# Performance work log

Measured on AMD Instinct MI355X. Metric: run time of the kernel, lower is better.

## Reference

```python
import jax, jax.numpy as jnp
import numpy as np
import math

B, L, HID = 2, 2048, 1024
NH, DH = 16, 64
MASK_VAL = -1000000000.0  # half_precision_flag == False


def setup_inputs() -> dict:
    key = jax.random.key(0)
    ks = jax.random.split(key, 12)
    s = 0.02
    return {
        "queries": jax.random.normal(ks[0], (B, L, HID), jnp.float32),
        "keys": jax.random.normal(ks[1], (B, L, HID), jnp.float32),
        "values": jax.random.normal(ks[2], (B, L, HID), jnp.float32),
        "mask": jax.random.randint(ks[3], (B, L, L), 0, 2, jnp.int32),
        "Wq": jax.random.normal(ks[4], (HID, NH * DH), jnp.float32) * s,
        "bq": jnp.zeros((NH * DH,), jnp.float32),
        "Wk": jax.random.normal(ks[5], (HID, NH * DH), jnp.float32) * s,
        "bk": jnp.zeros((NH * DH,), jnp.float32),
        "Wv": jax.random.normal(ks[6], (HID, NH * DH), jnp.float32) * s,
        "bv": jnp.zeros((NH * DH,), jnp.float32),
        "Wo": jax.random.normal(ks[7], (NH * DH, HID), jnp.float32) * s,
        "bo": jnp.zeros((HID,), jnp.float32),
    }


def reference(queries, keys, values, mask, Wq, bq, Wk, bk, Wv, bv, Wo, bo):
    # Linear projections: (B, L, NH*DH)
    q = queries @ Wq + bq
    k = keys @ Wk + bk
    v = values @ Wv + bv
    # FAITHFUL to original: raw .view(B, NH, -1, DH) without transpose
    q = q.reshape(B, NH, L, DH)
    k = k.reshape(B, NH, L, DH)
    v = v.reshape(B, NH, L, DH)
    # scaled dot-product scores: (B, NH, L, L)
    scores = jnp.einsum("bhqd,bhkd->bhqk", q, k) / math.sqrt(DH)
    scores = jnp.where(mask[:, None, :, :] == 0, MASK_VAL, scores)
    probs = jax.nn.softmax(scores, axis=-1)  # dropout p=0 -> identity
    ctx = jnp.einsum("bhqk,bhkd->bhqd", probs, v)  # (B, NH, L, DH)
    # transpose(1,2) then flatten heads, as in original
    ctx = ctx.transpose(0, 2, 1, 3).reshape(B, L, NH * DH)
    return ctx @ Wo + bo
```

## Files before the change

### kernel.cpp

```cpp
#include <hip/hip_runtime.h>
#include <stdint.h>

typedef __bf16 bf16;
typedef __bf16 bf16x8 __attribute__((ext_vector_type(8)));
typedef __bf16 bf16x4 __attribute__((ext_vector_type(4)));
typedef __bf16 bf16x2 __attribute__((ext_vector_type(2)));
typedef float  f32x4  __attribute__((ext_vector_type(4)));
typedef float  f32x16 __attribute__((ext_vector_type(16)));
typedef short  s16x4  __attribute__((ext_vector_type(4)));
typedef short  s16x8  __attribute__((ext_vector_type(8)));
typedef unsigned int u32x2 __attribute__((ext_vector_type(2)));
typedef unsigned int u32x4 __attribute__((ext_vector_type(4)));
typedef unsigned long long ull;

#define GLOAD16(gptr, lptr)                                                     \
  __builtin_amdgcn_global_load_lds(                                             \
      (const __attribute__((address_space(1))) void*)(gptr),                    \
      (__attribute__((address_space(3))) void*)(lptr), 16, 0, 0)

#define MFMA16(a, b, c) __builtin_amdgcn_mfma_f32_16x16x32_bf16((a), (b), (c), 0, 0, 0)
#define MFMA32(a, b, c) __builtin_amdgcn_mfma_f32_32x32x16_bf16((a), (b), (c), 0, 0, 0)

static constexpr int B_ = 2, L_ = 2048, NH_ = 16, DH_ = 64;
static constexpr float QSCALE = 0.18033688011112042f;

__global__ __launch_bounds__(256) void k_prep(const float* __restrict__ q,
                                              const float* __restrict__ k,
                                              const float* __restrict__ v,
                                              const int* __restrict__ mask,
                                              const float* __restrict__ wq,
                                              const float* __restrict__ wk,
                                              const float* __restrict__ wv,
                                              const float* __restrict__ wo,
                                              bf16* __restrict__ X,
                                              bf16* __restrict__ Wt,
                                              ull* __restrict__ mb) {
  __shared__ float t[32][33];
  const int bid = blockIdx.x, tid = threadIdx.x;
  if (bid < 32768) {
    int tt = bid * 256 + tid;
    ull bal = __ballot(mask[tt] != 0);
    if ((tid & 63) == 0) mb[tt >> 6] = bal;
  } else if (bid < 45056) {
    int u = bid - 32768;
    int z = u >> 12, x = u & 4095;
    const float* in = z == 0 ? q : (z == 1 ? k : v);
    bf16* out = X + (size_t)z * 4194304;
    int i = x * 256 + tid;
    const float4 f = ((const float4*)in)[i];
    bf16x4 o = {(bf16)f.x, (bf16)f.y, (bf16)f.z, (bf16)f.w};
    ((bf16x4*)out)[i] = o;
  } else {
    int u = bid - 45056;
    int z = u >> 10, rem = u & 1023;
    const float* in = z == 0 ? wq : (z == 1 ? wk : (z == 2 ? wv : wo));
    bf16* out = Wt + (size_t)z * 1048576;
    int bx = (rem & 31) * 32, by = (rem >> 5) * 32;
    int x = tid & 31, y = tid >> 5;
#pragma unroll
    for (int r = 0; r < 4; ++r)
      t[y + r * 8][x] = in[(size_t)(by + y + r * 8) * 1024 + bx + x];
    __syncthreads();
#pragma unroll
    for (int r = 0; r < 4; ++r)
      out[(size_t)(bx + y + r * 8) * 1024 + by + x] = (bf16)t[x][y + r * 8];
  }
}

__global__ __launch_bounds__(256) void k_gemm3(const bf16* __restrict__ Xb,
                                               const bf16* __restrict__ Wb,
                                               const float* __restrict__ b0,
                                               const float* __restrict__ b1,
                                               const float* __restrict__ b2,
                                               bf16* __restrict__ Ob) {
  const int z = blockIdx.z;
  const bf16* A  = Xb + (size_t)z * 4194304;
  const bf16* Bt = Wb + (size_t)z * 1048576;
  const float* bias = z == 0 ? b0 : (z == 1 ? b1 : b2);
  bf16* C = Ob + (size_t)z * 4194304;
  const int m0 = blockIdx.y * 128, n0 = blockIdx.x * 128;
  __shared__ __align__(16) bf16 As[128 * 32];
  __shared__ __align__(16) bf16 Bs[128 * 32];
  const int tid = threadIdx.x, lane = tid & 63, w = tid >> 6, quad = lane >> 4, l15 = lane & 15;
  const int wm = (w & 1) * 64, wn = (w >> 1) * 64;
  f32x4 acc[4][4] = {};
  for (int kt = 0; kt < 32; ++kt) {
    const int kk = kt * 32;
#pragma unroll
    for (int i = 0; i < 2; ++i) {
      int s = tid + i * 256;
      int r = s >> 2, c = (s & 3) ^ ((r >> 1) & 3);
      GLOAD16(A + (size_t)(m0 + r) * 1024 + kk + c * 8, As + s * 8);
      GLOAD16(Bt + (size_t)(n0 + r) * 1024 + kk + c * 8, Bs + s * 8);
    }
    __syncthreads();
    bf16x8 af[4], bb[4];
#pragma unroll
    for (int i = 0; i < 4; ++i) {
      int ra = wm + i * 16 + l15, rb = wn + i * 16 + l15;
      af[i] = *(const bf16x8*)(As + (ra * 4 + (quad ^ ((ra >> 1) & 3))) * 8);
      bb[i] = *(const bf16x8*)(Bs + (rb * 4 + (quad ^ ((rb >> 1) & 3))) * 8);
    }
#pragma unroll
    for (int mi = 0; mi < 4; ++mi)
#pragma unroll
      for (int ni = 0; ni < 4; ++ni)
        acc[mi][ni] = MFMA16(af[mi], bb[ni], acc[mi][ni]);
    __syncthreads();
  }
  const float scale = (z == 0) ? QSCALE : 1.0f;
#pragma unroll
  for (int mi = 0; mi < 4; ++mi)
#pragma unroll
    for (int ni = 0; ni < 4; ++ni) {
      int row = m0 + wm + mi * 16 + quad * 4;
      int col = n0 + wn + ni * 16 + l15;
      float bz = bias[col];
      if (z == 2) {
        int b_ = row >> 11, l = row & 2047;
        int hh = l >> 7;
        int i0 = (l & 127) * 16 + (col >> 6);
        int d  = col & 63;
        bf16* dst = C + (size_t)(b_ * 16 + hh) * 131072;
#pragma unroll
        for (int r = 0; r < 4; ++r) {
          int iK = i0 + 16 * r;
          dst[((size_t)(iK >> 3) * 64 + d) * 8 + (iK & 7)] = (bf16)(acc[mi][ni][r] + bz);
        }
      } else {
#pragma unroll
        for (int r = 0; r < 4; ++r)
          C[(size_t)(row + r) * 1024 + col] = (bf16)((acc[mi][ni][r] + bz) * scale);
      }
    }
}

__global__ __launch_bounds__(256) void k_gemmo(const bf16* __restrict__ A,
                                               const bf16* __restrict__ Bt,
                                               const float* __restrict__ bias,
                                               float* __restrict__ C) {
  const int m0 = blockIdx.y * 64, n0 = blockIdx.x * 128;
  __shared__ __align__(16) bf16 As[64 * 32];
  __shared__ __align__(16) bf16 Bs[128 * 32];
  const int tid = threadIdx.x, lane = tid & 63, w = tid >> 6, quad = lane >> 4, l15 = lane & 15;
  const int wn = w * 32;
  f32x4 acc[4][2] = {};
  for (int kt = 0; kt < 32; ++kt) {
    const int kk = kt * 32;
    {
      int r = tid >> 2, c = (tid & 3) ^ ((r >> 1) & 3);
      GLOAD16(A + (size_t)(m0 + r) * 1024 + kk + c * 8, As + tid * 8);
    }
#pragma unroll
    for (int i = 0; i < 2; ++i) {
      int s = tid + i * 256;
      int r = s >> 2, c = (s & 3) ^ ((r >> 1) & 3);
      GLOAD16(Bt + (size_t)(n0 + r) * 1024 + kk + c * 8, Bs + s * 8);
    }
    __syncthreads();
    bf16x8 af[4], bb[2];
#pragma unroll
    for (int i = 0; i < 4; ++i) {
      int ra = i * 16 + l15;
      af[i] = *(const bf16x8*)(As + (ra * 4 + (quad ^ ((ra >> 1) & 3))) * 8);
    }
#pragma unroll
    for (int i = 0; i < 2; ++i) {
      int rb = wn + i * 16 + l15;
      bb[i] = *(const bf16x8*)(Bs + (rb * 4 + (quad ^ ((rb >> 1) & 3))) * 8);
    }
#pragma unroll
    for (int mi = 0; mi < 4; ++mi)
#pragma unroll
      for (int ni = 0; ni < 2; ++ni)
        acc[mi][ni] = MFMA16(af[mi], bb[ni], acc[mi][ni]);
    __syncthreads();
  }
#pragma unroll
  for (int mi = 0; mi < 4; ++mi)
#pragma unroll
    for (int ni = 0; ni < 2; ++ni) {
      int row = m0 + mi * 16 + quad * 4;
      int col = n0 + wn + ni * 16 + l15;
      float bz = bias[col];
#pragma unroll
      for (int r = 0; r < 4; ++r)
        C[(size_t)(row + r) * 1024 + col] = acc[mi][ni][r] + bz;
    }
}

static __device__ __forceinline__ unsigned pack2(float a, float b) {
  bf16x2 t = {(bf16)a, (bf16)b};
  return __builtin_bit_cast(unsigned, t);
}

static __device__ __forceinline__ void flash_step(
    const bf16* __restrict__ Kc, const bf16* __restrict__ Vc, ull word,
    const bf16x8 (&qf)[4], bf16x8 ones8,
    int hi, int keyq, int vo0, int vo1, int vo2, int vo3,
    f32x16& accO0, f32x16& accO1, f32x16& accL) {
  bf16x8 v0 = *(const bf16x8*)(Vc + vo0);
  bf16x8 v1 = *(const bf16x8*)(Vc + vo1);
  bf16x8 v2 = *(const bf16x8*)(Vc + vo2);
  bf16x8 v3 = *(const bf16x8*)(Vc + vo3);

  f32x16 st = {};
  __builtin_amdgcn_s_setprio(1);
#pragma unroll
  for (int ks = 0; ks < 4; ++ks) {
    bf16x8 kf = *(const bf16x8*)(Kc + (keyq * 8 + ((ks * 2 + hi) ^ (keyq & 7))) * 8);
    st = MFMA32(kf, qf[ks], st);
  }
  __builtin_amdgcn_s_setprio(0);

  const unsigned w32 = (unsigned)(word >> ((keyq & 32) + 4 * hi));
#pragma unroll
  for (int r = 0; r < 16; ++r) {
    const int bit = (r >> 2) * 8 + (r & 3);
    st[r] = (w32 >> bit) & 1u ? __builtin_amdgcn_exp2f(st[r]) : 0.f;
  }

  bf16x8 af0, af1;
  {
    unsigned c0 = pack2(st[0], st[1]);
    unsigned c1 = pack2(st[2], st[3]);
    unsigned c2 = pack2(st[4], st[5]);
    unsigned c3 = pack2(st[6], st[7]);
    u32x2 s0 = __builtin_amdgcn_permlane32_swap(c0, c2, false, false);
    u32x2 s1 = __builtin_amdgcn_permlane32_swap(c1, c3, false, false);
    u32x4 a4 = {s0.x, s1.x, s0.y, s1.y};
    af0 = __builtin_bit_cast(bf16x8, a4);
    c0 = pack2(st[8], st[9]);
    c1 = pack2(st[10], st[11]);
    c2 = pack2(st[12], st[13]);
    c3 = pack2(st[14], st[15]);
    s0 = __builtin_amdgcn_permlane32_swap(c0, c2, false, false);
    s1 = __builtin_amdgcn_permlane32_swap(c1, c3, false, false);
    u32x4 b4 = {s0.x, s1.x, s0.y, s1.y};
    af1 = __builtin_bit_cast(bf16x8, b4);
  }

  __builtin_amdgcn_s_setprio(1);
  accL  = MFMA32(af0, ones8, accL);
  accL  = MFMA32(af1, ones8, accL);
  accO0 = MFMA32(af0, v0, accO0);
  accO1 = MFMA32(af0, v1, accO1);
  accO0 = MFMA32(af1, v2, accO0);
  accO1 = MFMA32(af1, v3, accO1);
  __builtin_amdgcn_s_setprio(0);
}

__global__ __launch_bounds__(512, 2) void k_flash(const bf16* __restrict__ Qp,
                                                  const bf16* __restrict__ Kp,
                                                  const bf16* __restrict__ Vtp,
                                                  const ull* __restrict__ mb,
                                                  bf16* __restrict__ ctx) {
  const int b = blockIdx.z, h = blockIdx.y, q0 = blockIdx.x * 128;
  const size_t HEAD = 131072;
  const bf16* Q  = Qp  + ((size_t)b * NH_ + h) * HEAD;
  const bf16* K  = Kp  + ((size_t)b * NH_ + h) * HEAD;
  const bf16* Vt = Vtp + ((size_t)b * NH_ + h) * HEAD;
  const ull* mrow = mb + (size_t)b * L_ * 32;

  __shared__ __align__(16) unsigned char RAW[65536];
  bf16* Ksb = (bf16*)RAW;
  bf16* Vsb = (bf16*)(RAW + 32768);

  const int tid = threadIdx.x, lane = tid & 63, w = tid >> 6;
  const int hi = lane >> 5, l31 = lane & 31;
  const int kh = w & 1, qq = w >> 1;
  const int keyq = kh * 32 + l31;
  const size_t mw = (size_t)(q0 + qq * 32 + l31) * 32;
  const int vo0 = ((kh * 4 + hi) * 64 + l31) * 8;
  const int vo1 = vo0 + 256;
  const int vo2 = vo0 + 1024;
  const int vo3 = vo2 + 256;

  bf16x8 qf[4];
  {
    const bf16* qrow = Q + (size_t)(q0 + qq * 32 + l31) * 64 + hi * 8;
    qf[0] = *(const bf16x8*)(qrow);
    qf[1] = *(const bf16x8*)(qrow + 16);
    qf[2] = *(const bf16x8*)(qrow + 32);
    qf[3] = *(const bf16x8*)(qrow + 48);
  }

  ull wa = mrow[mw + 0], wb2 = mrow[mw + 1], wc = mrow[mw + 2], wd;

#define STAGE(T, SL)                                                            \
  {                                                                             \
    int s_ = tid, key_ = s_ >> 3, c_ = (s_ & 7) ^ (key_ & 7);                   \
    GLOAD16(K + ((size_t)(T) * 64 + key_) * 64 + c_ * 8, Ksb + (SL) * 4096 + s_ * 8); \
    GLOAD16(Vt + (size_t)(T) * 4096 + s_ * 8, Vsb + (SL) * 4096 + s_ * 8);      \
  }
#define WB(N) asm volatile("s_waitcnt vmcnt(" #N ")\n\ts_barrier" ::: "memory")
#define STEP(SL, WORD)                                                          \
  flash_step(Ksb + (SL) * 4096, Vsb + (SL) * 4096, (WORD), qf, ones8, hi, keyq, \
             vo0, vo1, vo2, vo3, accO0, accO1, accL)

  STAGE(0, 0);
  STAGE(1, 1);
  STAGE(2, 2);

  f32x16 accO0 = {}, accO1 = {}, accL = {};
  const s16x8 one8s = {0x3F80, 0x3F80, 0x3F80, 0x3F80, 0x3F80, 0x3F80, 0x3F80, 0x3F80};
  const bf16x8 ones8 = __builtin_bit_cast(bf16x8, one8s);

  WB(4); wd  = mrow[mw + 3]; STAGE(3, 3); STEP(0, wa);
  WB(5); wa  = mrow[mw + 4]; STAGE(4, 0); STEP(1, wb2);
  WB(6); wb2 = mrow[mw + 5]; STAGE(5, 1); STEP(2, wc);
  WB(6); wc  = mrow[mw + 6]; STAGE(6, 2); STEP(3, wd);
  for (int g = 1; g < 7; ++g) {
    const int kt0 = g * 4;
    WB(6); wd  = mrow[mw + kt0 + 3]; STAGE(kt0 + 3, 3); STEP(0, wa);
    WB(6); wa  = mrow[mw + kt0 + 4]; STAGE(kt0 + 4, 0); STEP(1, wb2);
    WB(6); wb2 = mrow[mw + kt0 + 5]; STAGE(kt0 + 5, 1); STEP(2, wc);
    WB(6); wc  = mrow[mw + kt0 + 6]; STAGE(kt0 + 6, 2); STEP(3, wd);
  }
  WB(6); wd = mrow[mw + 31]; STAGE(31, 3); STEP(0, wa);
  WB(5); STEP(1, wb2);
  WB(3); STEP(2, wc);
  WB(0); STEP(3, wd);
#undef STEP
#undef WB
#undef STAGE

  __syncthreads();

  float* red  = (float*)RAW;
  float* redL = (float*)(RAW + 32768);
  if (kh == 1) {
#pragma unroll
    for (int r = 0; r < 16; ++r) {
      const int qrel = (r & 3) + 8 * (r >> 2) + 4 * hi;
      red[qq * 2048 + qrel * 64 + l31]      = accO0[r];
      red[qq * 2048 + qrel * 64 + 32 + l31] = accO1[r];
      if (l31 == 0) redL[qq * 32 + qrel] = accL[r];
    }
  }
  __syncthreads();
  if (kh == 0) {
#pragma unroll
    for (int r = 0; r < 16; ++r) {
      const int qrel = (r & 3) + 8 * (r >> 2) + 4 * hi;
      const float ls = accL[r] + redL[qq * 32 + qrel];
      const float rl = 1.0f / ls;
      const float o0 = accO0[r] + red[qq * 2048 + qrel * 64 + l31];
      const float o1 = accO1[r] + red[qq * 2048 + qrel * 64 + 32 + l31];
      const int rowg = q0 + qq * 32 + qrel;
      ctx[((size_t)b * L_ + rowg) * 1024 + h * 64 + l31]      = (bf16)(o0 * rl);
      ctx[((size_t)b * L_ + rowg) * 1024 + h * 64 + 32 + l31] = (bf16)(o1 * rl);
    }
  }
}

extern "C" void kernel_launch(void* const* d_in, const int* in_sizes, int n_in,
                              void* d_out, int out_size, void* d_ws, size_t ws_size,
                              hipStream_t stream) {
  (void)in_sizes; (void)n_in; (void)out_size; (void)ws_size;
  const float* q    = (const float*)d_in[0];
  const float* k    = (const float*)d_in[1];
  const float* v    = (const float*)d_in[2];
  const int*   mask = (const int*)d_in[3];
  const float* Wq = (const float*)d_in[4];
  const float* bq = (const float*)d_in[5];
  const float* Wk = (const float*)d_in[6];
  const float* bk = (const float*)d_in[7];
  const float* Wv = (const float*)d_in[8];
  const float* bv = (const float*)d_in[9];
  const float* Wo = (const float*)d_in[10];
  const float* bo = (const float*)d_in[11];
  float* out = (float*)d_out;

  char* ws = (char*)d_ws;
  const size_t SX = (size_t)4096 * 1024 * 2;
  const size_t SW = (size_t)1024 * 1024 * 2;
  bf16* X   = (bf16*)(ws);
  bf16* Wt  = (bf16*)(ws + 3 * SX);
  bf16* QKV = (bf16*)(ws + 3 * SX + 4 * SW);
  bf16* Qp  = QKV;
  bf16* Kp  = QKV + 4194304;
  bf16* Vtp = QKV + 2 * 4194304;
  bf16* Ctx = (bf16*)(ws + 6 * SX + 4 * SW);
  ull* mbits = (ull*)(ws + 7 * SX + 4 * SW);

  dim3 blk(256);
  k_prep<<<49152, blk, 0, stream>>>(q, k, v, mask, Wq, Wk, Wv, Wo, X, Wt, mbits);

  k_gemm3<<<dim3(8, 32, 3), blk, 0, stream>>>(X, Wt, bq, bk, bv, QKV);

  k_flash<<<dim3(16, NH_, B_), dim3(512), 0, stream>>>(Qp, Kp, Vtp, mbits, Ctx);

  k_gemmo<<<dim3(8, 64), blk, 0, stream>>>(Ctx, Wt + 3 * 1048576, bo, out);
}
```

Baseline: 275.8 us.

## Shrink flash blocks to 64 queries, double-buffer K/V, stage mask bits in LDS

The flash kernel now runs 256-thread blocks over 64 query rows, twice as many blocks, with a two-slot K/V pipeline in place of the four-slot vmcnt-scheduled one. Mask words are loaded into shared memory by one wave instead of per-lane global reads, and the K swizzle changes to spread bank accesses. The prep kernel merges work so each block handles several tiles, cutting the grid from 49152 blocks to 5120. The aim is higher occupancy and less block launch overhead, but the shallower prefetch and a full barrier on every tile may expose more memory latency.

```diff
diff --git a/kernel.cpp b/kernel.cpp
--- a/kernel.cpp
+++ b/kernel.cpp
@@ -37,33 +37,44 @@
                                               ull* __restrict__ mb) {
   __shared__ float t[32][33];
   const int bid = blockIdx.x, tid = threadIdx.x;
-  if (bid < 32768) {
-    int tt = bid * 256 + tid;
-    ull bal = __ballot(mask[tt] != 0);
-    if ((tid & 63) == 0) mb[tt >> 6] = bal;
-  } else if (bid < 45056) {
-    int u = bid - 32768;
-    int z = u >> 12, x = u & 4095;
-    const float* in = z == 0 ? q : (z == 1 ? k : v);
-    bf16* out = X + (size_t)z * 4194304;
-    int i = x * 256 + tid;
-    const float4 f = ((const float4*)in)[i];
-    bf16x4 o = {(bf16)f.x, (bf16)f.y, (bf16)f.z, (bf16)f.w};
-    ((bf16x4*)out)[i] = o;
+  if (bid < 2048) {
+#pragma unroll
+    for (int it = 0; it < 16; ++it) {
+      int tt = (bid * 16 + it) * 256 + tid;
+      ull bal = __ballot(mask[tt] != 0);
+      if ((tid & 63) == 0) mb[tt >> 6] = bal;
+    }
+  } else if (bid < 4096) {
+    const int u0 = (bid - 2048) * 6;
+#pragma unroll
+    for (int it = 0; it < 6; ++it) {
+      int u = u0 + it;
+      int z = u >> 12, x = u & 4095;
+      const float* in = z == 0 ? q : (z == 1 ? k : v);
+      bf16* out = X + (size_t)z * 4194304;
+      int i = x * 256 + tid;
+      const float4 f = ((const float4*)in)[i];
+      bf16x4 o = {(bf16)f.x, (bf16)f.y, (bf16)f.z, (bf16)f.w};
+      ((bf16x4*)out)[i] = o;
+    }
   } else {
-    int u = bid - 45056;
-    int z = u >> 10, rem = u & 1023;
-    const float* in = z == 0 ? wq : (z == 1 ? wk : (z == 2 ? wv : wo));
-    bf16* out = Wt + (size_t)z * 1048576;
-    int bx = (rem & 31) * 32, by = (rem >> 5) * 32;
-    int x = tid & 31, y = tid >> 5;
-#pragma unroll
-    for (int r = 0; r < 4; ++r)
-      t[y + r * 8][x] = in[(size_t)(by + y + r * 8) * 1024 + bx + x];
-    __syncthreads();
-#pragma unroll
-    for (int r = 0; r < 4; ++r)
-      out[(size_t)(bx + y + r * 8) * 1024 + by + x] = (bf16)t[x][y + r * 8];
+    const int t0 = (bid - 4096) * 4;
+    for (int it = 0; it < 4; ++it) {
+      int u = t0 + it;
+      int z = u >> 10, rem = u & 1023;
+      const float* in = z == 0 ? wq : (z == 1 ? wk : (z == 2 ? wv : wo));
+      bf16* out = Wt + (size_t)z * 1048576;
+      int bx = (rem & 31) * 32, by = (rem >> 5) * 32;
+      int x = tid & 31, y = tid >> 5;
+#pragma unroll
+      for (int r = 0; r < 4; ++r)
+        t[y + r * 8][x] = in[(size_t)(by + y + r * 8) * 1024 + bx + x];
+      __syncthreads();
+#pragma unroll
+      for (int r = 0; r < 4; ++r)
+        out[(size_t)(bx + y + r * 8) * 1024 + by + x] = (bf16)t[x][y + r * 8];
+      __syncthreads();
+    }
   }
 }
 
@@ -197,7 +208,7 @@
 static __device__ __forceinline__ void flash_step(
     const bf16* __restrict__ Kc, const bf16* __restrict__ Vc, ull word,
     const bf16x8 (&qf)[4], bf16x8 ones8,
-    int hi, int keyq, int vo0, int vo1, int vo2, int vo3,
+    int hi, int keyq, int swz, int vo0, int vo1, int vo2, int vo3,
     f32x16& accO0, f32x16& accO1, f32x16& accL) {
   bf16x8 v0 = *(const bf16x8*)(Vc + vo0);
   bf16x8 v1 = *(const bf16x8*)(Vc + vo1);
@@ -208,7 +219,7 @@
   __builtin_amdgcn_s_setprio(1);
 #pragma unroll
   for (int ks = 0; ks < 4; ++ks) {
-    bf16x8 kf = *(const bf16x8*)(Kc + (keyq * 8 + ((ks * 2 + hi) ^ (keyq & 7))) * 8);
+    bf16x8 kf = *(const bf16x8*)(Kc + (keyq * 8 + ((ks * 2 + hi) ^ swz)) * 8);
     st = MFMA32(kf, qf[ks], st);
   }
   __builtin_amdgcn_s_setprio(0);
@@ -250,27 +261,28 @@
   __builtin_amdgcn_s_setprio(0);
 }
 
-__global__ __launch_bounds__(512, 2) void k_flash(const bf16* __restrict__ Qp,
+__global__ __launch_bounds__(256, 4) void k_flash(const bf16* __restrict__ Qp,
                                                   const bf16* __restrict__ Kp,
                                                   const bf16* __restrict__ Vtp,
                                                   const ull* __restrict__ mb,
                                                   bf16* __restrict__ ctx) {
-  const int b = blockIdx.z, h = blockIdx.y, q0 = blockIdx.x * 128;
+  const int b = blockIdx.z, h = blockIdx.y, q0 = blockIdx.x * 64;
   const size_t HEAD = 131072;
   const bf16* Q  = Qp  + ((size_t)b * NH_ + h) * HEAD;
   const bf16* K  = Kp  + ((size_t)b * NH_ + h) * HEAD;
   const bf16* Vt = Vtp + ((size_t)b * NH_ + h) * HEAD;
   const ull* mrow = mb + (size_t)b * L_ * 32;
 
-  __shared__ __align__(16) unsigned char RAW[65536];
+  __shared__ __align__(16) unsigned char RAW[34816];
   bf16* Ksb = (bf16*)RAW;
-  bf16* Vsb = (bf16*)(RAW + 32768);
+  bf16* Vsb = (bf16*)(RAW + 16384);
+  ull*  Msb = (ull*)(RAW + 32768);
 
   const int tid = threadIdx.x, lane = tid & 63, w = tid >> 6;
   const int hi = lane >> 5, l31 = lane & 31;
   const int kh = w & 1, qq = w >> 1;
   const int keyq = kh * 32 + l31;
-  const size_t mw = (size_t)(q0 + qq * 32 + l31) * 32;
+  const int swz = (keyq ^ (keyq >> 3)) & 7;
   const int vo0 = ((kh * 4 + hi) * 64 + l31) * 8;
   const int vo1 = vo0 + 256;
   const int vo2 = vo0 + 1024;
@@ -285,50 +297,42 @@
     qf[3] = *(const bf16x8*)(qrow + 48);
   }
 
-  ull wa = mrow[mw + 0], wb2 = mrow[mw + 1], wc = mrow[mw + 2], wd;
-
 #define STAGE(T, SL)                                                            \
   {                                                                             \
-    int s_ = tid, key_ = s_ >> 3, c_ = (s_ & 7) ^ (key_ & 7);                   \
-    GLOAD16(K + ((size_t)(T) * 64 + key_) * 64 + c_ * 8, Ksb + (SL) * 4096 + s_ * 8); \
-    GLOAD16(Vt + (size_t)(T) * 4096 + s_ * 8, Vsb + (SL) * 4096 + s_ * 8);      \
-  }
-#define WB(N) asm volatile("s_waitcnt vmcnt(" #N ")\n\ts_barrier" ::: "memory")
-#define STEP(SL, WORD)                                                          \
-  flash_step(Ksb + (SL) * 4096, Vsb + (SL) * 4096, (WORD), qf, ones8, hi, keyq, \
-             vo0, vo1, vo2, vo3, accO0, accO1, accL)
+    _Pragma("unroll")                                                           \
+    for (int i_ = 0; i_ < 2; ++i_) {                                            \
+      int s_ = tid + i_ * 256;                                                  \
+      int key_ = s_ >> 3, c_ = (s_ & 7) ^ ((key_ ^ (key_ >> 3)) & 7);           \
+      GLOAD16(K + ((size_t)(T) * 64 + key_) * 64 + c_ * 8, Ksb + (SL) * 4096 + s_ * 8); \
+      GLOAD16(Vt + (size_t)(T) * 4096 + s_ * 8, Vsb + (SL) * 4096 + s_ * 8);    \
+    }                                                                           \
+  }
 
   STAGE(0, 0);
-  STAGE(1, 1);
-  STAGE(2, 2);
+  if (w == 0) GLOAD16(mrow + (size_t)(q0 + lane) * 32, (bf16*)Msb + lane * 8);
+  __syncthreads();
 
   f32x16 accO0 = {}, accO1 = {}, accL = {};
   const s16x8 one8s = {0x3F80, 0x3F80, 0x3F80, 0x3F80, 0x3F80, 0x3F80, 0x3F80, 0x3F80};
   const bf16x8 ones8 = __builtin_bit_cast(bf16x8, one8s);
 
-  WB(4); wd  = mrow[mw + 3]; STAGE(3, 3); STEP(0, wa);
-  WB(5); wa  = mrow[mw + 4]; STAGE(4, 0); STEP(1, wb2);
-  WB(6); wb2 = mrow[mw + 5]; STAGE(5, 1); STEP(2, wc);
-  WB(6); wc  = mrow[mw + 6]; STAGE(6, 2); STEP(3, wd);
-  for (int g = 1; g < 7; ++g) {
-    const int kt0 = g * 4;
-    WB(6); wd  = mrow[mw + kt0 + 3]; STAGE(kt0 + 3, 3); STEP(0, wa);
-    WB(6); wa  = mrow[mw + kt0 + 4]; STAGE(kt0 + 4, 0); STEP(1, wb2);
-    WB(6); wb2 = mrow[mw + kt0 + 5]; STAGE(kt0 + 5, 1); STEP(2, wc);
-    WB(6); wc  = mrow[mw + kt0 + 6]; STAGE(kt0 + 6, 2); STEP(3, wd);
-  }
-  WB(6); wd = mrow[mw + 31]; STAGE(31, 3); STEP(0, wa);
-  WB(5); STEP(1, wb2);
-  WB(3); STEP(2, wc);
-  WB(0); STEP(3, wd);
-#undef STEP
-#undef WB
+  for (int kt = 0; kt < 32; ++kt) {
+    const int cur = kt & 1;
+    if (kt + 1 < 32) {
+      STAGE(kt + 1, cur ^ 1);
+      if ((kt & 1) && w == 0)
+        GLOAD16(mrow + (size_t)(q0 + lane) * 32 + (kt + 1),
+                (bf16*)Msb + (((kt + 1) >> 1) & 1) * 512 + lane * 8);
+    }
+    const ull word = Msb[((kt >> 1) & 1) * 128 + (qq * 32 + l31) * 2 + cur];
+    flash_step(Ksb + cur * 4096, Vsb + cur * 4096, word, qf, ones8, hi, keyq, swz,
+               vo0, vo1, vo2, vo3, accO0, accO1, accL);
+    __syncthreads();
+  }
 #undef STAGE
 
-  __syncthreads();
-
   float* red  = (float*)RAW;
-  float* redL = (float*)(RAW + 32768);
+  float* redL = (float*)(RAW + 16384);
   if (kh == 1) {
 #pragma unroll
     for (int r = 0; r < 16; ++r) {
@@ -385,11 +389,11 @@
   ull* mbits = (ull*)(ws + 7 * SX + 4 * SW);
 
   dim3 blk(256);
-  k_prep<<<49152, blk, 0, stream>>>(q, k, v, mask, Wq, Wk, Wv, Wo, X, Wt, mbits);
+  k_prep<<<5120, blk, 0, stream>>>(q, k, v, mask, Wq, Wk, Wv, Wo, X, Wt, mbits);
 
   k_gemm3<<<dim3(8, 32, 3), blk, 0, stream>>>(X, Wt, bq, bk, bv, QKV);
 
-  k_flash<<<dim3(16, NH_, B_), dim3(512), 0, stream>>>(Qp, Kp, Vtp, mbits, Ctx);
+  k_flash<<<dim3(32, NH_, B_), blk, 0, stream>>>(Qp, Kp, Vtp, mbits, Ctx);
 
   k_gemmo<<<dim3(8, 64), blk, 0, stream>>>(Ctx, Wt + 3 * 1048576, bo, out);
 }
```

Measured after the change: 266.5 us. 3.4% less time.
